# Performance work log

Measured on AMD Instinct MI355X. Metric: run time of the kernel, lower is better.

The kernel has to match this reference:

```python
import jax, jax.numpy as jnp
import numpy as np

N = 50000      # nodes
E = 600000     # edges (before self-loops)
F = 128        # num_features
H = 8          # heads
C = 16         # hidden_dim (per-head channels)
D = H * C      # 128 = hidden_dim * heads
NEF = 4        # NUM_EDGE_FEATURES (polynomial pairwise features)
LN_EPS = 1e-5
LRELU_SLOPE = 0.2


def setup_inputs() -> dict:
    key = jax.random.key(0)
    ks = jax.random.split(key, 32)

    def nrm(k, shp, s=0.05):
        return jax.random.normal(k, shp, dtype=jnp.float32) * s

    return {
        "x": jax.random.normal(ks[0], (N, F), dtype=jnp.float32),
        "edge_index": jax.random.randint(ks[1], (2, E), 0, N),
        # edge encoder: Linear(NEF,16) -> ReLU -> Linear(16,H)
        "enc_w1": nrm(ks[2], (C, NEF)), "enc_b1": jnp.zeros((C,), jnp.float32),
        "enc_w2": nrm(ks[3], (H, C)),   "enc_b2": jnp.zeros((H,), jnp.float32),
        # input projection Linear(F, D)
        "in_w": nrm(ks[4], (D, F)), "in_b": jnp.zeros((D,), jnp.float32),
        # conv1 (GATConv F -> C, heads=H, edge_dim=H)
        "lin_w1": nrm(ks[5], (D, F)),
        "att_src1": nrm(ks[6], (H, C)), "att_dst1": nrm(ks[7], (H, C)), "att_edge1": nrm(ks[8], (H, C)),
        "lin_edge_w1": nrm(ks[9], (D, H)), "bias1": jnp.zeros((D,), jnp.float32),
        # conv2 (GATConv D -> C, heads=H, edge_dim=H)
        "lin_w2": nrm(ks[10], (D, D)),
        "att_src2": nrm(ks[11], (H, C)), "att_dst2": nrm(ks[12], (H, C)), "att_edge2": nrm(ks[13], (H, C)),
        "lin_edge_w2": nrm(ks[14], (D, H)), "bias2": jnp.zeros((D,), jnp.float32),
        # layer norms
        "g1": jnp.ones((D,), jnp.float32), "bn1": jnp.zeros((D,), jnp.float32),
        "g2": jnp.ones((D,), jnp.float32), "bn2": jnp.zeros((D,), jnp.float32),
        # JK projection Linear(3D, D)
        "jk_w": nrm(ks[15], (D, 3 * D)), "jk_b": jnp.zeros((D,), jnp.float32),
    }


def _layer_norm(h, g, b):
    mu = jnp.mean(h, axis=-1, keepdims=True)
    var = jnp.var(h, axis=-1, keepdims=True)
    return (h - mu) * jax.lax.rsqrt(var + LN_EPS) * g + b


def _edge_features(x, src, dst):
    # polynomial pairwise features: dot, squared distance, squared norms
    xi, xj = x[src], x[dst]                       # [E,F]
    return jnp.stack([
        jnp.sum(xi * xj, -1),
        jnp.sum((xi - xj) ** 2, -1),
        jnp.sum(xi * xi, -1),
        jnp.sum(xj * xj, -1),
    ], axis=-1)                                   # [E,NEF]


def _gat_conv(x, src, dst, edge_attr, lin_w, att_src, att_dst, att_edge,
              lin_edge_w, bias):
    """PyG GATConv, concat=True, edge_dim=H, eval mode (no dropout)."""
    xs = (x @ lin_w.T).reshape(N, H, C)                      # [N,H,C]
    a_src = jnp.sum(xs * att_src, -1)                        # [N,H]
    a_dst = jnp.sum(xs * att_dst, -1)                        # [N,H]
    e = (edge_attr @ lin_edge_w.T).reshape(-1, H, C)         # [E+N,H,C]
    a_edge = jnp.sum(e * att_edge, -1)                       # [E+N,H]
    alpha = a_src[src] + a_dst[dst] + a_edge                 # [E+N,H]
    alpha = jnp.where(alpha > 0, alpha, LRELU_SLOPE * alpha)
    # segment softmax over destination nodes (every node has a self-loop)
    m = jax.ops.segment_max(alpha, dst, num_segments=N)
    alpha = jnp.exp(alpha - m[dst])
    denom = jax.ops.segment_sum(alpha, dst, num_segments=N)
    alpha = alpha / (denom[dst] + 1e-16)
    msg = xs[src] * alpha[..., None]                         # [E+N,H,C]
    out = jax.ops.segment_sum(msg, dst, num_segments=N)      # [N,H,C]
    return out.reshape(N, D) + bias


def reference(x, edge_index, enc_w1, enc_b1, enc_w2, enc_b2, in_w, in_b,
              lin_w1, att_src1, att_dst1, att_edge1, lin_edge_w1, bias1,
              lin_w2, att_src2, att_dst2, att_edge2, lin_edge_w2, bias2,
              g1, bn1, g2, bn2, jk_w, jk_b):
    src, dst = edge_index[0], edge_index[1]
    # edge encoder
    ef = _edge_features(x, src, dst)                         # [E,NEF]
    ea = jax.nn.relu(ef @ enc_w1.T + enc_b1) @ enc_w2.T + enc_b2  # [E,H]
    # add self-loops with fill_value='mean' edge_attr (PyG default)
    loop = jnp.arange(N)
    src_f = jnp.concatenate([src, loop])
    dst_f = jnp.concatenate([dst, loop])
    ea_f = jnp.concatenate([ea, jnp.broadcast_to(jnp.mean(ea, 0), (N, H))])

    h0 = x @ in_w.T + in_b                                   # [N,D]
    h1 = jax.nn.elu(_gat_conv(x, src_f, dst_f, ea_f, lin_w1, att_src1,
                              att_dst1, att_edge1, lin_edge_w1, bias1))
    h1 = _layer_norm(h1 + h0, g1, bn1)
    h2 = jax.nn.elu(_gat_conv(h1, src_f, dst_f, ea_f, lin_w2, att_src2,
                              att_dst2, att_edge2, lin_edge_w2, bias2))
    h2 = _layer_norm(h2 + h1, g2, bn2)
    h = jnp.concatenate([h0, h1, h2], axis=-1)               # [N,3D]
    return h @ jk_w.T + jk_b                                 # [N,D]
```

## Files before the change

kernel.cpp:

```cpp
#include <hip/hip_runtime.h>

#define NN 50000
#define EE 600000
#define FF 128
#define HH 8
#define CC 16
#define DD 128
#define EPAD 950272
#define NBLK 196

typedef unsigned short u16;
typedef _Float16 h2t __attribute__((ext_vector_type(2)));
typedef _Float16 h8 __attribute__((ext_vector_type(8)));
typedef float f4 __attribute__((ext_vector_type(4)));

#if defined(__has_builtin)
#if __has_builtin(__builtin_amdgcn_fdot2)
#define HAS_FDOT2 1
#endif
#endif

static __device__ __forceinline__ float h2f(u16 u) {
    _Float16 h; __builtin_memcpy(&h, &u, 2); return (float)h;
}
static __device__ __forceinline__ u16 f2h(float f) {
    _Float16 h = (_Float16)f; u16 u; __builtin_memcpy(&u, &h, 2); return u;
}
static __device__ __forceinline__ float lo2f(unsigned x) { return h2f((u16)(x & 0xffff)); }
static __device__ __forceinline__ float hi2f(unsigned x) { return h2f((u16)(x >> 16)); }

static __device__ __forceinline__ float dot8(uint4 a, uint4 b, float c) {
#ifdef HAS_FDOT2
    h2t ax[4], bx[4];
    __builtin_memcpy(&ax, &a, 16); __builtin_memcpy(&bx, &b, 16);
    c = __builtin_amdgcn_fdot2(ax[0], bx[0], c, false);
    c = __builtin_amdgcn_fdot2(ax[1], bx[1], c, false);
    c = __builtin_amdgcn_fdot2(ax[2], bx[2], c, false);
    c = __builtin_amdgcn_fdot2(ax[3], bx[3], c, false);
#else
    c += lo2f(a.x) * lo2f(b.x) + hi2f(a.x) * hi2f(b.x)
       + lo2f(a.y) * lo2f(b.y) + hi2f(a.y) * hi2f(b.y)
       + lo2f(a.z) * lo2f(b.z) + hi2f(a.z) * hi2f(b.z)
       + lo2f(a.w) * lo2f(b.w) + hi2f(a.w) * hi2f(b.w);
#endif
    return c;
}

static __device__ __forceinline__ int tswz(int row, int u) {
    return (row * 16 + (u ^ (row & 7))) * 8;
}

#define NBP 12500
__global__ void k_prep(const float* __restrict__ x, float* __restrict__ norms,
                       u16* __restrict__ xb,
                       const float* __restrict__ s0, u16* __restrict__ d0,
                       const float* __restrict__ s1, u16* __restrict__ d1,
                       const float* __restrict__ s2, u16* __restrict__ d2,
                       const float* __restrict__ s3, u16* __restrict__ d3,
                       const float* __restrict__ lew1, const float* __restrict__ aew1,
                       const float* __restrict__ lew2, const float* __restrict__ aew2,
                       const float* __restrict__ enc_w2, const float* __restrict__ enc_b2,
                       float* __restrict__ P1, float* __restrict__ q1,
                       float* __restrict__ P2, float* __restrict__ q2,
                       const int* __restrict__ ei, int* __restrict__ deg) {
    __shared__ float sM1[64], sM2[64];
    int bb = blockIdx.x;
    int t = threadIdx.x;
    if (bb < NBP) {
        int wid = t >> 6, lane = t & 63;
        int row = bb * 4 + wid;
        float2 v = ((const float2*)(x + (size_t)row * FF))[lane];
        float s = v.x * v.x + v.y * v.y;
        #pragma unroll
        for (int off = 1; off < 64; off <<= 1) s += __shfl_xor(s, off, 64);
        if (lane == 0) norms[row] = s;
        unsigned pk = (unsigned)f2h(v.x) | ((unsigned)f2h(v.y) << 16);
        *(unsigned*)(xb + (size_t)row * FF + lane * 2) = pk;
    } else if (bb < NBP + 48) {
        int b = bb - NBP;
        const float* s; u16* d; int base;
        if (b < 8)       { s = s0; d = d0; base = b * 2048; }
        else if (b < 16) { s = s1; d = d1; base = (b - 8) * 2048; }
        else if (b < 24) { s = s2; d = d2; base = (b - 16) * 2048; }
        else             { s = s3; d = d3; base = (b - 24) * 2048; }
        int i = base + t * 8;
        float4 v0 = *(const float4*)(s + i);
        float4 v1 = *(const float4*)(s + i + 4);
        u16 o[8] = {f2h(v0.x), f2h(v0.y), f2h(v0.z), f2h(v0.w),
                    f2h(v1.x), f2h(v1.y), f2h(v1.z), f2h(v1.w)};
        *(uint4*)(d + i) = *(uint4*)o;
    } else if (bb == NBP + 48) {
        if (t < 128) {
            int kk = (t & 63) >> 3, h = t & 7;
            const float* lew = (t < 64) ? lew1 : lew2;
            const float* ae  = (t < 64) ? aew1 : aew2;
            float s = 0.f;
            for (int c = 0; c < 16; ++c) s += lew[(h * 16 + c) * 8 + kk] * ae[h * 16 + c];
            if (t < 64) sM1[kk * 8 + h] = s; else sM2[kk * 8 + h] = s;
        }
        __syncthreads();
        if (t < 128) {
            int c = t >> 3, h = t & 7;
            float p1 = 0.f, p2 = 0.f;
            for (int k = 0; k < 8; ++k) {
                float w = enc_w2[k * 16 + c];
                p1 += w * sM1[k * 8 + h];
                p2 += w * sM2[k * 8 + h];
            }
            P1[c * 8 + h] = p1;
            P2[c * 8 + h] = p2;
            if (t < 8) {
                float x1 = 0.f, x2 = 0.f;
                for (int k = 0; k < 8; ++k) { float b = enc_b2[k]; x1 += b * sM1[k * 8 + t]; x2 += b * sM2[k * 8 + t]; }
                q1[t] = x1; q2[t] = x2;
            }
        }
    } else {
        int e = (bb - NBP - 49) * 256 + t;
        if (e < EE) atomicAdd(&deg[ei[EE + e]], 1);
    }
}

__global__ void k_scan1(const int* __restrict__ deg, int* __restrict__ bsum) {
    int t = threadIdx.x, wid = t >> 6, lane = t & 63;
    int i = blockIdx.x * 256 + t;
    int v = (i < NN) ? ((deg[i] + 7) & ~7) : 0;
    #pragma unroll
    for (int off = 1; off < 64; off <<= 1) v += __shfl_xor(v, off, 64);
    __shared__ int ws[4];
    if (lane == 0) ws[wid] = v;
    __syncthreads();
    if (t == 0) bsum[blockIdx.x] = ws[0] + ws[1] + ws[2] + ws[3];
}

__global__ void k_scan2(int* __restrict__ bsum, int* __restrict__ rp) {
    int t = threadIdx.x, wid = t >> 6, lane = t & 63;
    int v = (t < NBLK) ? bsum[t] : 0;
    int sc = v;
    #pragma unroll
    for (int off = 1; off < 64; off <<= 1) { int n = __shfl_up(sc, off, 64); if (lane >= off) sc += n; }
    __shared__ int ws[4], wso[4];
    if (lane == 63) ws[wid] = sc;
    __syncthreads();
    if (t == 0) {
        int c = 0;
        for (int k = 0; k < 4; ++k) { wso[k] = c; c += ws[k]; }
        rp[NN] = c;
    }
    __syncthreads();
    if (t < NBLK) bsum[t] = sc - v + wso[wid];
}

__global__ void k_scan3(const int* __restrict__ deg, const int* __restrict__ bsum,
                        int* __restrict__ rp, int* __restrict__ cursor) {
    int t = threadIdx.x, wid = t >> 6, lane = t & 63;
    int i = blockIdx.x * 256 + t;
    int v = (i < NN) ? ((deg[i] + 7) & ~7) : 0;
    int sc = v;
    #pragma unroll
    for (int off = 1; off < 64; off <<= 1) { int n = __shfl_up(sc, off, 64); if (lane >= off) sc += n; }
    __shared__ int ws[4], wso[4];
    if (lane == 63) ws[wid] = sc;
    __syncthreads();
    if (t == 0) {
        int c = 0;
        for (int k = 0; k < 4; ++k) { wso[k] = c; c += ws[k]; }
    }
    __syncthreads();
    int ex = bsum[blockIdx.x] + wso[wid] + sc - v;
    if (i < NN) { rp[i] = ex; cursor[i] = ex; }
}

#define SCB 2344
__global__ void k_scatter(const int* __restrict__ ei, int* __restrict__ cursor,
                          const int* __restrict__ deg, const int* __restrict__ rp,
                          int* __restrict__ srt_src, int* __restrict__ srt_dst) {
    int bb = blockIdx.x;
    if (bb < SCB) {
        int e = bb * 256 + threadIdx.x;
        if (e < EE) {
            int d = ei[EE + e];
            int pos = atomicAdd(&cursor[d], 1);
            srt_src[pos] = ei[e];
            srt_dst[pos] = d;
        }
    } else {
        int i = (bb - SCB) * 256 + threadIdx.x;
        if (i < NN) {
            int start = rp[i] + deg[i], end = rp[i + 1];
            for (int p = start; p < end; ++p) { srt_src[p] = i; srt_dst[p] = -1; }
        }
        if (i == 0) {
            int ep = rp[NN];
            for (int k = 0; k < 24; ++k) { srt_src[ep + k] = 0; srt_dst[ep + k] = -1; }
        }
    }
}

__global__ void k_encoder(const u16* __restrict__ xb,
                          const int* __restrict__ srt_src, const int* __restrict__ srt_dst,
                          const float* __restrict__ norms,
                          const float* __restrict__ enc_w1, const float* __restrict__ enc_b1,
                          const float* __restrict__ P1, const float* __restrict__ q1,
                          const float* __restrict__ P2, const float* __restrict__ q2,
                          float* __restrict__ ae1out, float* __restrict__ ae2out,
                          const int* __restrict__ epad) {
    __shared__ float hidbuf[16][17];
    int t = threadIdx.x, eq = t >> 4, l = t & 15;
    int conv = l >> 3, h = l & 7;
    int EP = *epad;
    float w0 = enc_w1[l * 4 + 0], w1 = enc_w1[l * 4 + 1];
    float w2 = enc_w1[l * 4 + 2], w3 = enc_w1[l * 4 + 3];
    float cA = w0 - 2.f * w1, cB = w1 + w2, cC = w1 + w3, cb = enc_b1[l];
    const float* Ps = conv ? P2 : P1;
    float Preg[16];
    #pragma unroll
    for (int c = 0; c < 16; ++c) Preg[c] = Ps[c * 8 + h];
    float qreg = conv ? q2[h] : q1[h];
    float* outp = conv ? ae2out : ae1out;
    int e0 = blockIdx.x * 64 + eq;
    int ss[4], dc[4]; bool ok[4], inr[4];
    #pragma unroll
    for (int j = 0; j < 4; ++j) {
        int e = e0 + j * 16;
        inr[j] = e < EP;
        int eidx = inr[j] ? e : 0;
        int d_ = srt_dst[eidx];
        ss[j] = srt_src[eidx];
        ok[j] = inr[j] && (d_ >= 0);
        dc[j] = d_ >= 0 ? d_ : ss[j];
    }
    float ni[4], nj[4];
    #pragma unroll
    for (int j = 0; j < 4; ++j) { ni[j] = norms[ss[j]]; nj[j] = norms[dc[j]]; }
    uint4 avA = *(const uint4*)(xb + (size_t)ss[0] * FF + l * 8);
    uint4 bvA = *(const uint4*)(xb + (size_t)dc[0] * FF + l * 8);
    uint4 avB = *(const uint4*)(xb + (size_t)ss[1] * FF + l * 8);
    uint4 bvB = *(const uint4*)(xb + (size_t)dc[1] * FF + l * 8);
    #pragma unroll
    for (int j = 0; j < 4; ++j) {
        uint4 av = (j & 1) ? avB : avA;
        uint4 bv = (j & 1) ? bvB : bvA;
        if (j + 2 < 4) {
            if (j & 1) { avB = *(const uint4*)(xb + (size_t)ss[j + 2] * FF + l * 8);
                         bvB = *(const uint4*)(xb + (size_t)dc[j + 2] * FF + l * 8); }
            else       { avA = *(const uint4*)(xb + (size_t)ss[j + 2] * FF + l * 8);
                         bvA = *(const uint4*)(xb + (size_t)dc[j + 2] * FF + l * 8); }
        }
        float dot = dot8(av, bv, 0.f);
        #pragma unroll
        for (int off = 1; off < 16; off <<= 1) dot += __shfl_xor(dot, off, 64);
        float v = cA * dot + cB * ni[j] + cC * nj[j] + cb;
        hidbuf[eq][l] = v > 0.f ? v : 0.f;
        float a = qreg;
        #pragma unroll
        for (int c = 0; c < 16; ++c) a += hidbuf[eq][c] * Preg[c];
        if (inr[j]) outp[(size_t)(e0 + j * 16) * 8 + h] = ok[j] ? a : 0.f;
    }
}

__global__ void k_redsum(const float* __restrict__ a1, const float* __restrict__ a2,
                         float* __restrict__ sums, unsigned* __restrict__ done,
                         float* __restrict__ se1, float* __restrict__ se2,
                         const int* __restrict__ epad) {
    int tid = threadIdx.x;
    int nf4 = (*epad) * 2;
    int gid = blockIdx.x * 256 + tid;
    int stride = gridDim.x * 256;
    float4 c1 = make_float4(0.f, 0.f, 0.f, 0.f), c2 = c1;
    for (int i = gid; i < nf4; i += stride) {
        float4 v1 = ((const float4*)a1)[i];
        float4 v2 = ((const float4*)a2)[i];
        c1.x += v1.x; c1.y += v1.y; c1.z += v1.z; c1.w += v1.w;
        c2.x += v2.x; c2.y += v2.y; c2.z += v2.z; c2.w += v2.w;
    }
    #pragma unroll
    for (int off = 2; off < 64; off <<= 1) {
        c1.x += __shfl_xor(c1.x, off, 64); c1.y += __shfl_xor(c1.y, off, 64);
        c1.z += __shfl_xor(c1.z, off, 64); c1.w += __shfl_xor(c1.w, off, 64);
        c2.x += __shfl_xor(c2.x, off, 64); c2.y += __shfl_xor(c2.y, off, 64);
        c2.z += __shfl_xor(c2.z, off, 64); c2.w += __shfl_xor(c2.w, off, 64);
    }
    __shared__ float b1[4][8], b2[4][8];
    int wid = tid >> 6, lane = tid & 63;
    if (lane < 2) {
        int hb = lane * 4;
        b1[wid][hb + 0] = c1.x; b1[wid][hb + 1] = c1.y; b1[wid][hb + 2] = c1.z; b1[wid][hb + 3] = c1.w;
        b2[wid][hb + 0] = c2.x; b2[wid][hb + 1] = c2.y; b2[wid][hb + 2] = c2.z; b2[wid][hb + 3] = c2.w;
    }
    __syncthreads();
    if (tid < 8) {
        float t1 = b1[0][tid] + b1[1][tid] + b1[2][tid] + b1[3][tid];
        float t2 = b2[0][tid] + b2[1][tid] + b2[2][tid] + b2[3][tid];
        atomicAdd(&sums[tid], t1);
        atomicAdd(&sums[8 + tid], t2);
    }
    __syncthreads();
    if (tid == 0) {
        __threadfence();
        unsigned old = atomicAdd(done, 1u);
        if (old == (unsigned)gridDim.x - 1u) {
            __threadfence();
            for (int hh = 0; hh < 8; ++hh) {
                float v1 = atomicAdd(&sums[hh], 0.f);
                float v2 = atomicAdd(&sums[8 + hh], 0.f);
                se1[hh] = v1 * (1.f / (float)EE);
                se2[hh] = v2 * (1.f / (float)EE);
            }
        }
    }
}

static __device__ __forceinline__ void att_epilogue(const f4 (&acc)[2][8],
        const float* __restrict__ att_src, const float* __restrict__ att_dst,
        float* __restrict__ a_src, float* __restrict__ a_dst,
        int r0, int w, int lr, int lk, int nrows) {
    float attS[8], attD[8];
    #pragma unroll
    for (int n = 0; n < 8; ++n) { attS[n] = att_src[n * 16 + lr]; attD[n] = att_dst[n * 16 + lr]; }
    int hh = lr & 7;
    #pragma unroll
    for (int m = 0; m < 2; ++m) {
        #pragma unroll
        for (int g = 0; g < 4; ++g) {
            float sv[8], dv[8];
            #pragma unroll
            for (int n = 0; n < 8; ++n) { float p = acc[m][n][g]; sv[n] = p * attS[n]; dv[n] = p * attD[n]; }
            #pragma unroll
            for (int off = 1; off < 16; off <<= 1) {
                #pragma unroll
                for (int n = 0; n < 8; ++n) {
                    sv[n] += __shfl_xor(sv[n], off, 64);
                    dv[n] += __shfl_xor(dv[n], off, 64);
                }
            }
            float so = lr < 8 ? sv[0] : dv[0];
            #pragma unroll
            for (int n = 1; n < 8; ++n) { float c = lr < 8 ? sv[n] : dv[n]; so = (hh == n) ? c : so; }
            int row = r0 + w * 32 + m * 16 + lk * 4 + g;
            if (row < nrows) {
                float* p = lr < 8 ? a_src : a_dst;
                p[(size_t)row * 8 + hh] = so;
            }
        }
    }
}

template <bool BIAS, bool ATT>
__global__ __launch_bounds__(256, 2) void k_mfma(const u16* __restrict__ X,
                                                 const u16* __restrict__ W,
                                                 const float* __restrict__ bias,
                                                 u16* __restrict__ out,
                                                 const float* __restrict__ att_src,
                                                 const float* __restrict__ att_dst,
                                                 float* __restrict__ a_src,
                                                 float* __restrict__ a_dst, int nrows) {
    __shared__ __align__(16) u16 tA[128 * 128];
    __shared__ __align__(16) u16 tB[128 * 128];
    int t = threadIdx.x;
    int r0 = blockIdx.x * 128;
    #pragma unroll
    for (int it = 0; it < 8; ++it) {
        int idx = it * 256 + t;
        int r = idx >> 4, u = idx & 15;
        uint4 v = make_uint4(0u, 0u, 0u, 0u);
        if (r0 + r < nrows) v = *(const uint4*)(X + (size_t)(r0 + r) * 128 + u * 8);
        *(uint4*)&tA[tswz(r, u)] = v;
        uint4 wv = *(const uint4*)(W + (size_t)r * 128 + u * 8);
        *(uint4*)&tB[tswz(r, u)] = wv;
    }
    __syncthreads();
    int l = t & 63, w = t >> 6;
    int lr = l & 15, lk = l >> 4;
    f4 acc[2][8];
    #pragma unroll
    for (int m = 0; m < 2; ++m)
        #pragma unroll
        for (int n = 0; n < 8; ++n) acc[m][n] = (f4){0.f, 0.f, 0.f, 0.f};
    #pragma unroll
    for (int s = 0; s < 4; ++s) {
        int u = s * 4 + lk;
        h8 a0 = *(h8*)&tA[tswz(w * 32 + lr, u)];
        h8 a1 = *(h8*)&tA[tswz(w * 32 + 16 + lr, u)];
        #pragma unroll
        for (int n = 0; n < 8; ++n) {
            h8 b = *(h8*)&tB[tswz(n * 16 + lr, u)];
            acc[0][n] = __builtin_amdgcn_mfma_f32_16x16x32_f16(a0, b, acc[0][n], 0, 0, 0);
            acc[1][n] = __builtin_amdgcn_mfma_f32_16x16x32_f16(a1, b, acc[1][n], 0, 0, 0);
        }
    }
    #pragma unroll
    for (int n = 0; n < 8; ++n) {
        int col = n * 16 + lr;
        float bv = BIAS ? bias[col] : 0.f;
        #pragma unroll
        for (int m = 0; m < 2; ++m) {
            #pragma unroll
            for (int g = 0; g < 4; ++g) {
                int row = r0 + w * 32 + m * 16 + lk * 4 + g;
                if (row < nrows) out[(size_t)row * 128 + col] = f2h(acc[m][n][g] + bv);
            }
        }
    }
    if (ATT) att_epilogue(acc, att_src, att_dst, a_src, a_dst, r0, w, lr, lk, nrows);
}

__global__ __launch_bounds__(256, 2) void k_mfma_x2(const u16* __restrict__ X,
                                                    const u16* __restrict__ W0,
                                                    const float* __restrict__ b0,
                                                    const u16* __restrict__ W1,
                                                    u16* __restrict__ out0,
                                                    u16* __restrict__ out1,
                                                    const float* __restrict__ att_src,
                                                    const float* __restrict__ att_dst,
                                                    float* __restrict__ a_src,
                                                    float* __restrict__ a_dst, int nrows) {
    __shared__ __align__(16) u16 tA[128 * 128];
    __shared__ __align__(16) u16 tB[128 * 128];
    int t = threadIdx.x;
    int r0 = blockIdx.x * 128;
    #pragma unroll
    for (int it = 0; it < 8; ++it) {
        int idx = it * 256 + t;
        int r = idx >> 4, u = idx & 15;
        uint4 v = make_uint4(0u, 0u, 0u, 0u);
        if (r0 + r < nrows) v = *(const uint4*)(X + (size_t)(r0 + r) * 128 + u * 8);
        *(uint4*)&tA[tswz(r, u)] = v;
        uint4 wv = *(const uint4*)(W0 + (size_t)r * 128 + u * 8);
        *(uint4*)&tB[tswz(r, u)] = wv;
    }
    __syncthreads();
    int l = t & 63, w = t >> 6;
    int lr = l & 15, lk = l >> 4;
    f4 acc[2][8];
    #pragma unroll
    for (int m = 0; m < 2; ++m)
        #pragma unroll
        for (int n = 0; n < 8; ++n) acc[m][n] = (f4){0.f, 0.f, 0.f, 0.f};
    #pragma unroll
    for (int s = 0; s < 4; ++s) {
        int u = s * 4 + lk;
        h8 a0 = *(h8*)&tA[tswz(w * 32 + lr, u)];
        h8 a1 = *(h8*)&tA[tswz(w * 32 + 16 + lr, u)];
        #pragma unroll
        for (int n = 0; n < 8; ++n) {
            h8 b = *(h8*)&tB[tswz(n * 16 + lr, u)];
            acc[0][n] = __builtin_amdgcn_mfma_f32_16x16x32_f16(a0, b, acc[0][n], 0, 0, 0);
            acc[1][n] = __builtin_amdgcn_mfma_f32_16x16x32_f16(a1, b, acc[1][n], 0, 0, 0);
        }
    }
    #pragma unroll
    for (int n = 0; n < 8; ++n) {
        int col = n * 16 + lr;
        float bv = b0[col];
        #pragma unroll
        for (int m = 0; m < 2; ++m)
            #pragma unroll
            for (int g = 0; g < 4; ++g) {
                int row = r0 + w * 32 + m * 16 + lk * 4 + g;
                if (row < nrows) out0[(size_t)row * 128 + col] = f2h(acc[m][n][g] + bv);
            }
    }
    __syncthreads();
    #pragma unroll
    for (int it = 0; it < 8; ++it) {
        int idx = it * 256 + t;
        int r = idx >> 4, u = idx & 15;
        uint4 wv = *(const uint4*)(W1 + (size_t)r * 128 + u * 8);
        *(uint4*)&tB[tswz(r, u)] = wv;
    }
    __syncthreads();
    #pragma unroll
    for (int m = 0; m < 2; ++m)
        #pragma unroll
        for (int n = 0; n < 8; ++n) acc[m][n] = (f4){0.f, 0.f, 0.f, 0.f};
    #pragma unroll
    for (int s = 0; s < 4; ++s) {
        int u = s * 4 + lk;
        h8 a0 = *(h8*)&tA[tswz(w * 32 + lr, u)];
        h8 a1 = *(h8*)&tA[tswz(w * 32 + 16 + lr, u)];
        #pragma unroll
        for (int n = 0; n < 8; ++n) {
            h8 b = *(h8*)&tB[tswz(n * 16 + lr, u)];
            acc[0][n] = __builtin_amdgcn_mfma_f32_16x16x32_f16(a0, b, acc[0][n], 0, 0, 0);
            acc[1][n] = __builtin_amdgcn_mfma_f32_16x16x32_f16(a1, b, acc[1][n], 0, 0, 0);
        }
    }
    #pragma unroll
    for (int n = 0; n < 8; ++n) {
        int col = n * 16 + lr;
        #pragma unroll
        for (int m = 0; m < 2; ++m)
            #pragma unroll
            for (int g = 0; g < 4; ++g) {
                int row = r0 + w * 32 + m * 16 + lk * 4 + g;
                if (row < nrows) out1[(size_t)row * 128 + col] = f2h(acc[m][n][g]);
            }
    }
    att_epilogue(acc, att_src, att_dst, a_src, a_dst, r0, w, lr, lk, nrows);
}

__global__ __launch_bounds__(256, 2) void k_mfma_jk(const u16* __restrict__ h0,
                                                    const u16* __restrict__ h1,
                                                    const u16* __restrict__ h2,
                                                    const u16* __restrict__ W,
                                                    const float* __restrict__ bias,
                                                    float* __restrict__ out, int nrows) {
    __shared__ __align__(16) u16 tA[128 * 128];
    __shared__ __align__(16) u16 tB[128 * 128];
    int t = threadIdx.x;
    int r0 = blockIdx.x * 128;
    int l = t & 63, w = t >> 6;
    int lr = l & 15, lk = l >> 4;
    f4 acc[2][8];
    #pragma unroll
    for (int m = 0; m < 2; ++m)
        #pragma unroll
        for (int n = 0; n < 8; ++n) acc[m][n] = (f4){0.f, 0.f, 0.f, 0.f};
    for (int seg = 0; seg < 3; ++seg) {
        if (seg) __syncthreads();
        const u16* X = seg == 0 ? h0 : (seg == 1 ? h1 : h2);
        #pragma unroll
        for (int it = 0; it < 8; ++it) {
            int idx = it * 256 + t;
            int r = idx >> 4, u = idx & 15;
            uint4 v = make_uint4(0u, 0u, 0u, 0u);
            if (r0 + r < nrows) v = *(const uint4*)(X + (size_t)(r0 + r) * 128 + u * 8);
            *(uint4*)&tA[tswz(r, u)] = v;
            uint4 wv = *(const uint4*)(W + (size_t)r * 384 + seg * 128 + u * 8);
            *(uint4*)&tB[tswz(r, u)] = wv;
        }
        __syncthreads();
        #pragma unroll
        for (int s = 0; s < 4; ++s) {
            int u = s * 4 + lk;
            h8 a0 = *(h8*)&tA[tswz(w * 32 + lr, u)];
            h8 a1 = *(h8*)&tA[tswz(w * 32 + 16 + lr, u)];
            #pragma unroll
            for (int n = 0; n < 8; ++n) {
                h8 b = *(h8*)&tB[tswz(n * 16 + lr, u)];
                acc[0][n] = __builtin_amdgcn_mfma_f32_16x16x32_f16(a0, b, acc[0][n], 0, 0, 0);
                acc[1][n] = __builtin_amdgcn_mfma_f32_16x16x32_f16(a1, b, acc[1][n], 0, 0, 0);
            }
        }
    }
    #pragma unroll
    for (int n = 0; n < 8; ++n) {
        int col = n * 16 + lr;
        float bv = bias[col];
        #pragma unroll
        for (int m = 0; m < 2; ++m) {
            #pragma unroll
            for (int g = 0; g < 4; ++g) {
                int row = r0 + w * 32 + m * 16 + lk * 4 + g;
                if (row < nrows) out[(size_t)row * 128 + col] = acc[m][n][g] + bv;
            }
        }
    }
}

__global__ void k_weights(const int* __restrict__ srt_src, const int* __restrict__ srt_dst,
                          const float* __restrict__ ae, const float* __restrict__ a_src,
                          const float* __restrict__ a_dst, float* __restrict__ w,
                          const int* __restrict__ epad) {
    int pos = blockIdx.x * 256 + threadIdx.x;
    if (pos >= *epad) return;
    float* wp = w + (size_t)pos * 8;
    int d = srt_dst[pos];
    if (d < 0) {
        *(float4*)wp = make_float4(0.f, 0.f, 0.f, 0.f);
        *(float4*)(wp + 4) = make_float4(0.f, 0.f, 0.f, 0.f);
        return;
    }
    int s = srt_src[pos];
    const float* as = a_src + (size_t)s * 8;
    const float* ad = a_dst + (size_t)d * 8;
    const float* av = ae + (size_t)pos * 8;
    float4 s0 = *(const float4*)as, s1 = *(const float4*)(as + 4);
    float4 d0 = *(const float4*)ad, d1 = *(const float4*)(ad + 4);
    float4 e0 = *(const float4*)av, e1 = *(const float4*)(av + 4);
    float al[8] = {s0.x + d0.x + e0.x, s0.y + d0.y + e0.y, s0.z + d0.z + e0.z, s0.w + d0.w + e0.w,
                   s1.x + d1.x + e1.x, s1.y + d1.y + e1.y, s1.z + d1.z + e1.z, s1.w + d1.w + e1.w};
    float o[8];
    #pragma unroll
    for (int h = 0; h < 8; ++h) {
        float a = al[h];
        a = a > 0.f ? a : 0.2f * a;
        o[h] = __expf(a);
    }
    *(float4*)wp = make_float4(o[0], o[1], o[2], o[3]);
    *(float4*)(wp + 4) = make_float4(o[4], o[5], o[6], o[7]);
}

#define LDS4(S_, base_) { \
    _Pragma("unroll") \
    for (int k = 0; k < 4; ++k) S_[k] = srt_src[(base_) + k]; }

#define LDWX(W_, X_, S_, base_) { \
    _Pragma("unroll") \
    for (int k = 0; k < 4; ++k) { \
        W_[k] = wq[(size_t)((base_) + k) * 8 + h]; \
        X_[k] = *(const unsigned*)(xs + (size_t)S_[k] * 128 + lane * 2); } }

#define CP(W_, X_) { \
    _Pragma("unroll") \
    for (int k = 0; k < 4; ++k) { \
        float wc = W_[k]; unsigned xv = X_[k]; \
        acc0 += wc * lo2f(xv); \
        acc1 += wc * hi2f(xv); \
        denom += wc; } }

__global__ __launch_bounds__(256) void k_agg(const int* __restrict__ rp,
                      const int* __restrict__ srt_src,
                      const float* __restrict__ wq,
                      const float* __restrict__ a_src, const float* __restrict__ a_dst,
                      const float* __restrict__ se,
                      const u16* __restrict__ xs, const u16* __restrict__ res,
                      const float* __restrict__ bias, const float* __restrict__ gamma,
                      const float* __restrict__ beta, u16* __restrict__ outh) {
    int wv_ = threadIdx.x >> 6, lane = threadIdx.x & 63;
    int i = blockIdx.x * 4 + wv_;
    if (i >= NN) return;
    int h = lane >> 3;
    int b0 = rp[i], en = rp[i + 1];
    float acc0 = 0.f, acc1 = 0.f, denom = 0.f;
    if (b0 < en) {
        int SA[4], SB[4];
        float WA[4], WB[4]; unsigned XA[4], XB[4];
        LDS4(SA, b0)
        LDS4(SB, b0 + 4)
        LDWX(WA, XA, SA, b0)
        LDWX(WB, XB, SB, b0 + 4)
        LDS4(SA, b0 + 8)
        LDS4(SB, b0 + 12)
        for (int base = b0; base < en; base += 8) {
            CP(WA, XA)
            LDWX(WA, XA, SA, base + 8)
            LDS4(SA, base + 16)
            CP(WB, XB)
            LDWX(WB, XB, SB, base + 12)
            LDS4(SB, base + 20)
        }
    }
    {
        float al = a_src[i * 8 + h] + a_dst[i * 8 + h] + se[h];
        al = al > 0.f ? al : 0.2f * al;
        float wc = __expf(al);
        unsigned xv = *(const unsigned*)(xs + (size_t)i * 128 + lane * 2);
        denom += wc;
        acc0 += wc * lo2f(xv);
        acc1 += wc * hi2f(xv);
    }
    float inv = 1.f / (denom + 1e-16f);
    float2 bi = *(const float2*)(bias + lane * 2);
    float v0 = acc0 * inv + bi.x;
    float v1 = acc1 * inv + bi.y;
    v0 = v0 > 0.f ? v0 : (__expf(v0) - 1.f);
    v1 = v1 > 0.f ? v1 : (__expf(v1) - 1.f);
    unsigned rv = *(const unsigned*)(res + (size_t)i * 128 + lane * 2);
    v0 += lo2f(rv);
    v1 += hi2f(rv);
    float s = v0 + v1, q = v0 * v0 + v1 * v1;
    #pragma unroll
    for (int off = 1; off < 64; off <<= 1) { s += __shfl_xor(s, off, 64); q += __shfl_xor(q, off, 64); }
    float mu = s * (1.f / 128.f);
    float var = q * (1.f / 128.f) - mu * mu;
    float r = rsqrtf(var + 1e-5f);
    float2 ga = *(const float2*)(gamma + lane * 2);
    float2 be = *(const float2*)(beta + lane * 2);
    float o0 = (v0 - mu) * r * ga.x + be.x;
    float o1 = (v1 - mu) * r * ga.y + be.y;
    unsigned ov = (unsigned)f2h(o0) | ((unsigned)f2h(o1) << 16);
    *(unsigned*)(outh + (size_t)i * 128 + lane * 2) = ov;
}

extern "C" void kernel_launch(void* const* d_in, const int* in_sizes, int n_in,
                              void* d_out, int out_size, void* d_ws, size_t ws_size,
                              hipStream_t stream) {
    const float* x        = (const float*)d_in[0];
    const int*   ei       = (const int*)d_in[1];
    const float* enc_w1   = (const float*)d_in[2];
    const float* enc_b1   = (const float*)d_in[3];
    const float* enc_w2   = (const float*)d_in[4];
    const float* enc_b2   = (const float*)d_in[5];
    const float* in_w     = (const float*)d_in[6];
    const float* in_b     = (const float*)d_in[7];
    const float* lin_w1   = (const float*)d_in[8];
    const float* att_src1 = (const float*)d_in[9];
    const float* att_dst1 = (const float*)d_in[10];
    const float* att_edge1= (const float*)d_in[11];
    const float* lin_ew1  = (const float*)d_in[12];
    const float* bias1    = (const float*)d_in[13];
    const float* lin_w2   = (const float*)d_in[14];
    const float* att_src2 = (const float*)d_in[15];
    const float* att_dst2 = (const float*)d_in[16];
    const float* att_edge2= (const float*)d_in[17];
    const float* lin_ew2  = (const float*)d_in[18];
    const float* bias2    = (const float*)d_in[19];
    const float* g1       = (const float*)d_in[20];
    const float* bn1      = (const float*)d_in[21];
    const float* g2       = (const float*)d_in[22];
    const float* bn2      = (const float*)d_in[23];
    const float* jk_w     = (const float*)d_in[24];
    const float* jk_b     = (const float*)d_in[25];
    float* out = (float*)d_out;

    char* wsp = (char*)d_ws;
    size_t off = 0;
    auto alloc = [&](size_t bytes) -> char* {
        char* p = wsp + off;
        off += (bytes + 255) & ~(size_t)255;
        return p;
    };
    u16* x_bf   = (u16*)alloc(sizeof(u16) * (size_t)NN * 128);
    u16* h0b    = (u16*)alloc(sizeof(u16) * (size_t)NN * 128);
    u16* h1b    = (u16*)alloc(sizeof(u16) * (size_t)NN * 128);
    u16* h2b    = (u16*)alloc(sizeof(u16) * (size_t)NN * 128);
    u16* xsb    = (u16*)alloc(sizeof(u16) * (size_t)NN * 128);
    u16* inw_b  = (u16*)alloc(sizeof(u16) * 16384);
    u16* w1_b   = (u16*)alloc(sizeof(u16) * 16384);
    u16* w2_b   = (u16*)alloc(sizeof(u16) * 16384);
    u16* jkw_b  = (u16*)alloc(sizeof(u16) * 49152);
    float* ae1   = (float*)alloc(sizeof(float) * (size_t)EPAD * 8);
    float* ae2   = (float*)alloc(sizeof(float) * (size_t)EPAD * 8);
    float* wbuf  = (float*)alloc(sizeof(float) * (size_t)EPAD * 8);
    float* norms = (float*)alloc(sizeof(float) * NN);
    float* a_src1= (float*)alloc(sizeof(float) * NN * 8);
    float* a_dst1= (float*)alloc(sizeof(float) * NN * 8);
    float* a_src2= (float*)alloc(sizeof(float) * NN * 8);
    float* a_dst2= (float*)alloc(sizeof(float) * NN * 8);
    float* P1    = (float*)alloc(sizeof(float) * 128);
    float* q1    = (float*)alloc(sizeof(float) * 8);
    float* P2    = (float*)alloc(sizeof(float) * 128);
    float* q2    = (float*)alloc(sizeof(float) * 8);
    float* se1   = (float*)alloc(sizeof(float) * 8);
    float* se2   = (float*)alloc(sizeof(float) * 8);
    int* deg     = (int*)alloc(sizeof(int) * NN);
    float* sums  = (float*)alloc(sizeof(float) * 16);
    unsigned* done = (unsigned*)alloc(sizeof(unsigned));
    int* rp      = (int*)alloc(sizeof(int) * (NN + 1));
    int* cursor  = (int*)alloc(sizeof(int) * NN);
    int* bsum    = (int*)alloc(sizeof(int) * NBLK);
    int* srt_src = (int*)alloc(sizeof(int) * EPAD);
    int* srt_dst = (int*)alloc(sizeof(int) * EPAD);
    (void)ws_size; (void)in_sizes; (void)n_in; (void)out_size;
    const int* epad_ptr = rp + NN;

    hipMemsetAsync(deg, 0, (size_t)((char*)rp - (char*)deg), stream);

    k_prep<<<NBP + 48 + 1 + (EE + 255) / 256, 256, 0, stream>>>(
        x, norms, x_bf,
        in_w, inw_b, lin_w1, w1_b, lin_w2, w2_b, jk_w, jkw_b,
        lin_ew1, att_edge1, lin_ew2, att_edge2, enc_w2, enc_b2, P1, q1, P2, q2,
        ei, deg);
    k_scan1<<<NBLK, 256, 0, stream>>>(deg, bsum);
    k_scan2<<<1, 256, 0, stream>>>(bsum, rp);
    k_scan3<<<NBLK, 256, 0, stream>>>(deg, bsum, rp, cursor);
    k_scatter<<<SCB + (NN + 255) / 256, 256, 0, stream>>>(ei, cursor, deg, rp, srt_src, srt_dst);
    k_encoder<<<(EPAD + 63) / 64, 256, 0, stream>>>(x_bf, srt_src, srt_dst, norms, enc_w1, enc_b1,
                                                    P1, q1, P2, q2, ae1, ae2, epad_ptr);
    k_redsum<<<512, 256, 0, stream>>>(ae1, ae2, sums, done, se1, se2, epad_ptr);

    int gm = (NN + 127) / 128;
    int gw = (EPAD + 255) / 256;
    k_mfma_x2<<<gm, 256, 0, stream>>>(x_bf, inw_b, in_b, w1_b, h0b, xsb,
                                      att_src1, att_dst1, a_src1, a_dst1, NN);
    k_weights<<<gw, 256, 0, stream>>>(srt_src, srt_dst, ae1, a_src1, a_dst1, wbuf, epad_ptr);
    k_agg<<<(NN + 3) / 4, 256, 0, stream>>>(rp, srt_src, wbuf, a_src1, a_dst1, se1,
                                            xsb, h0b, bias1, g1, bn1, h1b);
    k_mfma<false, true><<<gm, 256, 0, stream>>>(h1b, w2_b, nullptr, xsb,
                                                att_src2, att_dst2, a_src2, a_dst2, NN);
    k_weights<<<gw, 256, 0, stream>>>(srt_src, srt_dst, ae2, a_src2, a_dst2, wbuf, epad_ptr);
    k_agg<<<(NN + 3) / 4, 256, 0, stream>>>(rp, srt_src, wbuf, a_src2, a_dst2, se2,
                                            xsb, h1b, bias2, g2, bn2, h2b);
    k_mfma_jk<<<gm, 256, 0, stream>>>(h0b, h1b, h2b, jkw_b, jk_b, out, NN);
}
```

Baseline: 342.5 us.

## Fuse attention-weight computation into aggregation and drop the edge weight buffer

Removes the separate k_weights pass. Each aggregation wave now computes the leaky-relu and exp attention weights on the fly from the edge encoder output, a_src and a_dst, spreading them across lanes with shuffles and masking self-loop padding slots via deg. The aggregation loop is restructured to process blocks of 8 edges with double buffering. The encoder skips the x gathers for padding edges, and the scatter zeroes the tail of the encoder buffers. This avoids writing and re-reading an EPAD×8 float buffer twice. In exchange, each aggregation block does more gather and exp work per edge.

```diff
diff --git a/kernel.cpp b/kernel.cpp
--- a/kernel.cpp
+++ b/kernel.cpp
@@ -174,7 +174,8 @@
 #define SCB 2344
 __global__ void k_scatter(const int* __restrict__ ei, int* __restrict__ cursor,
                           const int* __restrict__ deg, const int* __restrict__ rp,
-                          int* __restrict__ srt_src, int* __restrict__ srt_dst) {
+                          int* __restrict__ srt_src, int* __restrict__ srt_dst,
+                          float* __restrict__ ae1, float* __restrict__ ae2) {
     int bb = blockIdx.x;
     if (bb < SCB) {
         int e = bb * 256 + threadIdx.x;
@@ -193,6 +194,7 @@
         if (i == 0) {
             int ep = rp[NN];
             for (int k = 0; k < 24; ++k) { srt_src[ep + k] = 0; srt_dst[ep + k] = -1; }
+            for (int k = 0; k < 192; ++k) { ae1[(size_t)ep * 8 + k] = 0.f; ae2[(size_t)ep * 8 + k] = 0.f; }
         }
     }
 }
@@ -230,24 +232,22 @@
         ok[j] = inr[j] && (d_ >= 0);
         dc[j] = d_ >= 0 ? d_ : ss[j];
     }
+    uint4 av[4], bv[4];
     float ni[4], nj[4];
     #pragma unroll
-    for (int j = 0; j < 4; ++j) { ni[j] = norms[ss[j]]; nj[j] = norms[dc[j]]; }
-    uint4 avA = *(const uint4*)(xb + (size_t)ss[0] * FF + l * 8);
-    uint4 bvA = *(const uint4*)(xb + (size_t)dc[0] * FF + l * 8);
-    uint4 avB = *(const uint4*)(xb + (size_t)ss[1] * FF + l * 8);
-    uint4 bvB = *(const uint4*)(xb + (size_t)dc[1] * FF + l * 8);
-    #pragma unroll
     for (int j = 0; j < 4; ++j) {
-        uint4 av = (j & 1) ? avB : avA;
-        uint4 bv = (j & 1) ? bvB : bvA;
-        if (j + 2 < 4) {
-            if (j & 1) { avB = *(const uint4*)(xb + (size_t)ss[j + 2] * FF + l * 8);
-                         bvB = *(const uint4*)(xb + (size_t)dc[j + 2] * FF + l * 8); }
-            else       { avA = *(const uint4*)(xb + (size_t)ss[j + 2] * FF + l * 8);
-                         bvA = *(const uint4*)(xb + (size_t)dc[j + 2] * FF + l * 8); }
-        }
-        float dot = dot8(av, bv, 0.f);
+        if (ok[j]) {
+            av[j] = *(const uint4*)(xb + (size_t)ss[j] * FF + l * 8);
+            bv[j] = *(const uint4*)(xb + (size_t)dc[j] * FF + l * 8);
+            ni[j] = norms[ss[j]]; nj[j] = norms[dc[j]];
+        }
+    }
+    #pragma unroll
+    for (int j = 0; j < 4; ++j) {
+        if (!inr[j]) continue;
+        int e = e0 + j * 16;
+        if (!ok[j]) { outp[(size_t)e * 8 + h] = 0.f; continue; }
+        float dot = dot8(av[j], bv[j], 0.f);
         #pragma unroll
         for (int off = 1; off < 16; off <<= 1) dot += __shfl_xor(dot, off, 64);
         float v = cA * dot + cB * ni[j] + cC * nj[j] + cb;
@@ -255,7 +255,7 @@
         float a = qreg;
         #pragma unroll
         for (int c = 0; c < 16; ++c) a += hidbuf[eq][c] * Preg[c];
-        if (inr[j]) outp[(size_t)(e0 + j * 16) * 8 + h] = ok[j] ? a : 0.f;
+        outp[(size_t)e * 8 + h] = a;
     }
 }
 
@@ -559,60 +559,35 @@
     }
 }
 
-__global__ void k_weights(const int* __restrict__ srt_src, const int* __restrict__ srt_dst,
-                          const float* __restrict__ ae, const float* __restrict__ a_src,
-                          const float* __restrict__ a_dst, float* __restrict__ w,
-                          const int* __restrict__ epad) {
-    int pos = blockIdx.x * 256 + threadIdx.x;
-    if (pos >= *epad) return;
-    float* wp = w + (size_t)pos * 8;
-    int d = srt_dst[pos];
-    if (d < 0) {
-        *(float4*)wp = make_float4(0.f, 0.f, 0.f, 0.f);
-        *(float4*)(wp + 4) = make_float4(0.f, 0.f, 0.f, 0.f);
-        return;
-    }
-    int s = srt_src[pos];
-    const float* as = a_src + (size_t)s * 8;
-    const float* ad = a_dst + (size_t)d * 8;
-    const float* av = ae + (size_t)pos * 8;
-    float4 s0 = *(const float4*)as, s1 = *(const float4*)(as + 4);
-    float4 d0 = *(const float4*)ad, d1 = *(const float4*)(ad + 4);
-    float4 e0 = *(const float4*)av, e1 = *(const float4*)(av + 4);
-    float al[8] = {s0.x + d0.x + e0.x, s0.y + d0.y + e0.y, s0.z + d0.z + e0.z, s0.w + d0.w + e0.w,
-                   s1.x + d1.x + e1.x, s1.y + d1.y + e1.y, s1.z + d1.z + e1.z, s1.w + d1.w + e1.w};
-    float o[8];
-    #pragma unroll
-    for (int h = 0; h < 8; ++h) {
-        float a = al[h];
-        a = a > 0.f ? a : 0.2f * a;
-        o[h] = __expf(a);
-    }
-    *(float4*)wp = make_float4(o[0], o[1], o[2], o[3]);
-    *(float4*)(wp + 4) = make_float4(o[4], o[5], o[6], o[7]);
-}
-
-#define LDS4(S_, base_) { \
+#define LOADBLK(S_, W_, X_, base_) { \
     _Pragma("unroll") \
-    for (int k = 0; k < 4; ++k) S_[k] = srt_src[(base_) + k]; }
-
-#define LDWX(W_, X_, S_, base_) { \
+    for (int k = 0; k < 8; ++k) S_[k] = srt_src[(base_) + k]; \
+    float aev = ae[(size_t)(base_) * 8 + lane]; \
+    int sl = srt_src[(base_) + (lane >> 3)]; \
+    float asv = a_src[(size_t)sl * 8 + hw]; \
+    float alv = asv + adw + aev; \
+    alv = alv > 0.f ? alv : 0.2f * alv; \
+    float wvv = __expf(alv); \
     _Pragma("unroll") \
-    for (int k = 0; k < 4; ++k) { \
-        W_[k] = wq[(size_t)((base_) + k) * 8 + h]; \
-        X_[k] = *(const unsigned*)(xs + (size_t)S_[k] * 128 + lane * 2); } }
-
-#define CP(W_, X_) { \
+    for (int k = 0; k < 8; ++k) { \
+        float ww = __shfl(wvv, (k << 3) | h, 64); \
+        W_[k] = ((base_) + k < rend) ? ww : 0.f; } \
     _Pragma("unroll") \
-    for (int k = 0; k < 4; ++k) { \
+    for (int k = 0; k < 8; ++k) \
+        X_[k] = *(const unsigned*)(xs + (size_t)S_[k] * 128 + lane * 2); }
+
+#define CPBLK(W_, X_) { \
+    _Pragma("unroll") \
+    for (int k = 0; k < 8; ++k) { \
         float wc = W_[k]; unsigned xv = X_[k]; \
         acc0 += wc * lo2f(xv); \
         acc1 += wc * hi2f(xv); \
         denom += wc; } }
 
 __global__ __launch_bounds__(256) void k_agg(const int* __restrict__ rp,
+                      const int* __restrict__ deg,
                       const int* __restrict__ srt_src,
-                      const float* __restrict__ wq,
+                      const float* __restrict__ ae,
                       const float* __restrict__ a_src, const float* __restrict__ a_dst,
                       const float* __restrict__ se,
                       const u16* __restrict__ xs, const u16* __restrict__ res,
@@ -622,24 +597,23 @@
     int i = blockIdx.x * 4 + wv_;
     if (i >= NN) return;
     int h = lane >> 3;
-    int b0 = rp[i], en = rp[i + 1];
+    int hw = lane & 7;
+    int b0 = __builtin_amdgcn_readfirstlane(rp[i]);
+    int en = __builtin_amdgcn_readfirstlane(rp[i + 1]);
+    int rend = b0 + __builtin_amdgcn_readfirstlane(deg[i]);
+    float adw = a_dst[i * 8 + hw];
     float acc0 = 0.f, acc1 = 0.f, denom = 0.f;
     if (b0 < en) {
-        int SA[4], SB[4];
-        float WA[4], WB[4]; unsigned XA[4], XB[4];
-        LDS4(SA, b0)
-        LDS4(SB, b0 + 4)
-        LDWX(WA, XA, SA, b0)
-        LDWX(WB, XB, SB, b0 + 4)
-        LDS4(SA, b0 + 8)
-        LDS4(SB, b0 + 12)
-        for (int base = b0; base < en; base += 8) {
-            CP(WA, XA)
-            LDWX(WA, XA, SA, base + 8)
-            LDS4(SA, base + 16)
-            CP(WB, XB)
-            LDWX(WB, XB, SB, base + 12)
-            LDS4(SB, base + 20)
+        int SA[8], SB[8]; float WA[8], WB[8]; unsigned XA[8], XB[8];
+        int base = b0;
+        LOADBLK(SA, WA, XA, base)
+        while (true) {
+            LOADBLK(SB, WB, XB, base + 8)
+            CPBLK(WA, XA)
+            base += 8; if (base >= en) break;
+            LOADBLK(SA, WA, XA, base + 8)
+            CPBLK(WB, XB)
+            base += 8; if (base >= en) break;
         }
     }
     {
@@ -723,7 +697,6 @@
     u16* jkw_b  = (u16*)alloc(sizeof(u16) * 49152);
     float* ae1   = (float*)alloc(sizeof(float) * (size_t)EPAD * 8);
     float* ae2   = (float*)alloc(sizeof(float) * (size_t)EPAD * 8);
-    float* wbuf  = (float*)alloc(sizeof(float) * (size_t)EPAD * 8);
     float* norms = (float*)alloc(sizeof(float) * NN);
     float* a_src1= (float*)alloc(sizeof(float) * NN * 8);
     float* a_dst1= (float*)alloc(sizeof(float) * NN * 8);
@@ -756,22 +729,20 @@
     k_scan1<<<NBLK, 256, 0, stream>>>(deg, bsum);
     k_scan2<<<1, 256, 0, stream>>>(bsum, rp);
     k_scan3<<<NBLK, 256, 0, stream>>>(deg, bsum, rp, cursor);
-    k_scatter<<<SCB + (NN + 255) / 256, 256, 0, stream>>>(ei, cursor, deg, rp, srt_src, srt_dst);
+    k_scatter<<<SCB + (NN + 255) / 256, 256, 0, stream>>>(ei, cursor, deg, rp,
+                                                          srt_src, srt_dst, ae1, ae2);
     k_encoder<<<(EPAD + 63) / 64, 256, 0, stream>>>(x_bf, srt_src, srt_dst, norms, enc_w1, enc_b1,
                                                     P1, q1, P2, q2, ae1, ae2, epad_ptr);
     k_redsum<<<512, 256, 0, stream>>>(ae1, ae2, sums, done, se1, se2, epad_ptr);
 
     int gm = (NN + 127) / 128;
-    int gw = (EPAD + 255) / 256;
     k_mfma_x2<<<gm, 256, 0, stream>>>(x_bf, inw_b, in_b, w1_b, h0b, xsb,
                                       att_src1, att_dst1, a_src1, a_dst1, NN);
-    k_weights<<<gw, 256, 0, stream>>>(srt_src, srt_dst, ae1, a_src1, a_dst1, wbuf, epad_ptr);
-    k_agg<<<(NN + 3) / 4, 256, 0, stream>>>(rp, srt_src, wbuf, a_src1, a_dst1, se1,
+    k_agg<<<(NN + 3) / 4, 256, 0, stream>>>(rp, deg, srt_src, ae1, a_src1, a_dst1, se1,
                                             xsb, h0b, bias1, g1, bn1, h1b);
     k_mfma<false, true><<<gm, 256, 0, stream>>>(h1b, w2_b, nullptr, xsb,
                                                 att_src2, att_dst2, a_src2, a_dst2, NN);
-    k_weights<<<gw, 256, 0, stream>>>(srt_src, srt_dst, ae2, a_src2, a_dst2, wbuf, epad_ptr);
-    k_agg<<<(NN + 3) / 4, 256, 0, stream>>>(rp, srt_src, wbuf, a_src2, a_dst2, se2,
+    k_agg<<<(NN + 3) / 4, 256, 0, stream>>>(rp, deg, srt_src, ae2, a_src2, a_dst2, se2,
                                             xsb, h1b, bias2, g2, bn2, h2b);
     k_mfma_jk<<<gm, 256, 0, stream>>>(h0b, h1b, h2b, jkw_b, jk_b, out, NN);
 }
```

After: 317.9 us. 1.08x faster.
